# Kernel tuning notes

Measured on AMD Instinct MI355X. Metric: run time of the kernel, lower is better.

Reference implementation:

```python
import jax, jax.numpy as jnp
import numpy as np

B, T, C = 4, 2048, 768
N_HEAD = 12
HEAD_DIM = C // N_HEAD


def setup_inputs() -> dict:
    key = jax.random.key(0)
    k1, k2, k3 = jax.random.split(key, 3)
    x = jax.random.normal(k1, (B, T, C), dtype=jnp.float32)
    w_attn = jax.random.normal(k2, (C, 3 * C), dtype=jnp.float32) * (1.0 / np.sqrt(C))
    b_attn = jnp.zeros((3 * C,), dtype=jnp.float32)
    w_proj = jax.random.normal(k3, (C, C), dtype=jnp.float32) * (1.0 / np.sqrt(C))
    b_proj = jnp.zeros((C,), dtype=jnp.float32)
    return {"x": x, "w_attn": w_attn, "b_attn": b_attn, "w_proj": w_proj, "b_proj": b_proj}


def reference(x, w_attn, b_attn, w_proj, b_proj):
    # x: [B, T, C]
    Bs, Ts, Cs = x.shape
    qkv = x @ w_attn + b_attn                         # [B, T, 3C]
    q, k, v = jnp.split(qkv, 3, axis=-1)
    # -> [B, H, T, Dh]
    q = q.reshape(Bs, Ts, N_HEAD, HEAD_DIM).swapaxes(1, 2)
    k = k.reshape(Bs, Ts, N_HEAD, HEAD_DIM).swapaxes(1, 2)
    v = v.reshape(Bs, Ts, N_HEAD, HEAD_DIM).swapaxes(1, 2)
    scale = 1.0 / jnp.sqrt(jnp.asarray(HEAD_DIM, dtype=x.dtype))
    att = jnp.einsum('bhqd,bhkd->bhqk', q, k) * scale  # [B, H, T, T]
    causal = jnp.tril(jnp.ones((Ts, Ts), dtype=bool))[None, None]
    att = jnp.where(causal, att, jnp.asarray(-jnp.inf, dtype=att.dtype))
    att = jax.nn.softmax(att, axis=-1)
    y = jnp.einsum('bhqk,bhkd->bhqd', att, v)          # [B, H, T, Dh]
    y = y.swapaxes(1, 2).reshape(Bs, Ts, Cs)
    y = y @ w_proj + b_proj
    return y
```

## Files before the change

### kernel.cpp

```cpp
#include <hip/hip_runtime.h>
#include <cstdint>
#include <cstddef>

typedef __bf16 bf16x8 __attribute__((ext_vector_type(8)));
typedef float  f32x4  __attribute__((ext_vector_type(4)));
typedef unsigned short us;

#define DEV static __device__ __forceinline__

DEV us f2bf(float f) {
    unsigned int u = __builtin_bit_cast(unsigned int, f);
    u += 0x7FFFu + ((u >> 16) & 1u);
    return (us)(u >> 16);
}
DEV unsigned int pack2bf(float a, float b) {
    unsigned int ua = __builtin_bit_cast(unsigned int, a) + 0x8000u;
    unsigned int ub = __builtin_bit_cast(unsigned int, b) + 0x8000u;
    return (ua >> 16) | (ub & 0xFFFF0000u);
}

DEV void gll16(const void* g, void* l) {
    __builtin_amdgcn_global_load_lds(
        (const __attribute__((address_space(1))) unsigned int*)g,
        (__attribute__((address_space(3))) unsigned int*)l, 16, 0, 0);
}

DEV bf16x8 ld_frag(const us* p) {
    return __builtin_bit_cast(bf16x8, *reinterpret_cast<const uint4*>(p));
}

#define BB 4
#define TT 2048
#define CC 768
#define NH 12
#define DH 64
#define MM (BB*TT)
#define QSCALE 0.1803368801111144f

#define PREP_CAST_BLK 1024
#define PREP_TA_BLK   ((3*CC/32)*(CC/32))
#define PREP_TP_BLK   ((CC/32)*(CC/32))

__global__ __launch_bounds__(256)
void prep_k(const float* __restrict__ x, us* __restrict__ xb,
            const float* __restrict__ wA, us* __restrict__ wAt,
            const float* __restrict__ wP, us* __restrict__ wPt)
{
    const int bid = blockIdx.x;
    const int tid = threadIdx.x;

    if (bid < PREP_CAST_BLK) {
        const int n4 = MM * CC / 4;
        int i = bid * 256 + tid;
        const int stride = PREP_CAST_BLK * 256;
        for (; i < n4; i += stride) {
            float4 f = reinterpret_cast<const float4*>(x)[i];
            ushort4 o;
            o.x = f2bf(f.x); o.y = f2bf(f.y); o.z = f2bf(f.z); o.w = f2bf(f.w);
            reinterpret_cast<ushort4*>(xb)[i] = o;
        }
        return;
    }

    __shared__ float tile[32][33];
    const float* src; us* dst; int R, Cc, tb;
    if (bid < PREP_CAST_BLK + PREP_TA_BLK) {
        src = wA; dst = wAt; R = CC; Cc = 3 * CC; tb = bid - PREP_CAST_BLK;
    } else {
        src = wP; dst = wPt; R = CC; Cc = CC;     tb = bid - PREP_CAST_BLK - PREP_TA_BLK;
    }
    const int gx = Cc / 32;
    const int c0 = (tb % gx) * 32, r0 = (tb / gx) * 32;
    const int tx = tid & 31, ty = tid >> 5;
#pragma unroll
    for (int i = 0; i < 4; ++i)
        tile[ty + i*8][tx] = src[(size_t)(r0 + ty + i*8) * Cc + c0 + tx];
    __syncthreads();
#pragma unroll
    for (int i = 0; i < 4; ++i)
        dst[(size_t)(c0 + ty + i*8) * R + r0 + tx] = f2bf(tile[tx][ty + i*8]);
}


#define BM 128
#define BN 128
#define BK 32

template<int MODE>
__global__ __launch_bounds__(256)
void gemm_bt(const us* __restrict__ A,
             const us* __restrict__ Bt,
             const float* __restrict__ bias,
             float* __restrict__ Cout,
             us* __restrict__ Qo, us* __restrict__ Ko, us* __restrict__ Vo,
             int M, int N, int K)
{
    __shared__ __align__(16) us As[2][BM * BK];
    __shared__ __align__(16) us Bs[2][BN * BK];

    const int tid  = threadIdx.x;
    const int wave = tid >> 6, lane = tid & 63;
    const int quad = lane >> 4, l16 = lane & 15;
    const int waveM = (wave >> 1) * 64, waveN = (wave & 1) * 64;
    const int m0 = blockIdx.y * BM, n0 = blockIdx.x * BN;

    const f32x4 zero4 = {0.f, 0.f, 0.f, 0.f};
    f32x4 acc[4][4];
#pragma unroll
    for (int i = 0; i < 4; ++i)
#pragma unroll
        for (int j = 0; j < 4; ++j) acc[i][j] = zero4;

    const int lrow = lane >> 2, lch = (lane & 3) * 8;
    const int nk = K / BK;

    auto STAGE = [&](int buf, int kt) {
#pragma unroll
        for (int c = 0; c < 2; ++c) {
            int rb = (wave * 2 + c) * 16;
            int row = rb + lrow;
            gll16(A  + (size_t)(m0 + row) * K + kt * BK + lch, &As[buf][rb * BK]);
            gll16(Bt + (size_t)(n0 + row) * K + kt * BK + lch, &Bs[buf][rb * BK]);
        }
    };

    STAGE(0, 0);
    __syncthreads();
    int cur = 0;

    for (int kt = 0; kt < nk; ++kt) {
        if (kt + 1 < nk) STAGE(cur ^ 1, kt + 1);

        bf16x8 af[4], bfv[4];
#pragma unroll
        for (int mi = 0; mi < 4; ++mi)
            af[mi] = *reinterpret_cast<const bf16x8*>(&As[cur][(waveM + mi * 16 + l16) * BK + quad * 8]);
#pragma unroll
        for (int ni = 0; ni < 4; ++ni)
            bfv[ni] = *reinterpret_cast<const bf16x8*>(&Bs[cur][(waveN + ni * 16 + l16) * BK + quad * 8]);
#pragma unroll
        for (int mi = 0; mi < 4; ++mi)
#pragma unroll
            for (int ni = 0; ni < 4; ++ni)
                acc[mi][ni] = __builtin_amdgcn_mfma_f32_16x16x32_bf16(af[mi], bfv[ni], acc[mi][ni], 0, 0, 0);

        __syncthreads();
        cur ^= 1;
    }

#pragma unroll
    for (int mi = 0; mi < 4; ++mi) {
#pragma unroll
        for (int ni = 0; ni < 4; ++ni) {
            int n = n0 + waveN + ni * 16 + l16;
            float bv = bias[n];
            int mg = m0 + waveM + mi * 16 + quad * 4;
            if (MODE == 0) {
#pragma unroll
                for (int reg = 0; reg < 4; ++reg)
                    Cout[(size_t)(mg + reg) * N + n] = acc[mi][ni][reg] + bv;
            } else {
                int which = n / CC, c2 = n % CC;
                int h = c2 >> 6, d = c2 & 63;
                int b = mg >> 11, t0 = mg & 2047;
                size_t hb = (size_t)(b * NH + h) * TT * DH;
                if (which == 2) {
                    size_t off = hb + (size_t)(t0 >> 6) * 4096 + (d >> 4) * 1024
                               + ((t0 >> 3) & 7) * 128 + (d & 15) * 8 + (t0 & 7);
                    ushort4 pk;
                    pk.x = f2bf(acc[mi][ni][0] + bv);
                    pk.y = f2bf(acc[mi][ni][1] + bv);
                    pk.z = f2bf(acc[mi][ni][2] + bv);
                    pk.w = f2bf(acc[mi][ni][3] + bv);
                    *reinterpret_cast<ushort4*>(Vo + off) = pk;
                } else if (which == 1) {
                    size_t off = hb + (size_t)(t0 >> 4) * 1024 + (d >> 3) * 128
                               + (t0 & 15) * 8 + (d & 7);
#pragma unroll
                    for (int reg = 0; reg < 4; ++reg)
                        Ko[off + reg * 8] = f2bf(acc[mi][ni][reg] + bv);
                } else {
#pragma unroll
                    for (int reg = 0; reg < 4; ++reg) {
                        size_t off = hb + (size_t)(t0 + reg) * DH + d;
                        Qo[off] = f2bf((acc[mi][ni][reg] + bv) * QSCALE);
                    }
                }
            }
        }
    }
}

#define PST 72

__global__ __launch_bounds__(128)
void attn_k(const us* __restrict__ Qg,
            const us* __restrict__ Kg,
            const us* __restrict__ Vt,
            us* __restrict__ Og)
{
    __shared__ __align__(16) us Ps[2][32 * PST];

    const int tid  = threadIdx.x;
    const int wave = tid >> 6, lane = tid & 63;
    const int quad = lane >> 4, l16 = lane & 15;

    const int id  = blockIdx.x;
    const int xcd = id & 7, s = id >> 3;
    const int bh  = xcd + 8 * (s >> 4);
    const int q   = s & 15;
    const int pw  = 2 * q + wave;

    const size_t base = (size_t)bh * TT * DH;
    const int b = bh / NH, h = bh % NH;
    us* myP = Ps[wave];

    const f32x4 zero4 = {0.f, 0.f, 0.f, 0.f};

#pragma unroll 1
    for (int seg = 0; seg < 2; ++seg) {
        const int g   = seg ? 63 - pw : pw;
        const int nkt = (g >> 1) + 1;
        const int mA  = g * 32 + l16;
        const int mB  = mA + 16;

        bf16x8 qfA0 = ld_frag(Qg + base + (size_t)mA * DH + quad * 8);
        bf16x8 qfA1 = ld_frag(Qg + base + (size_t)mA * DH + 32 + quad * 8);
        bf16x8 qfB0 = ld_frag(Qg + base + (size_t)mB * DH + quad * 8);
        bf16x8 qfB1 = ld_frag(Qg + base + (size_t)mB * DH + 32 + quad * 8);

        f32x4 oA[4], oB[4];
#pragma unroll
        for (int i = 0; i < 4; ++i) { oA[i] = zero4; oB[i] = zero4; }
        float lrA = 0.f, lrB = 0.f;

#pragma unroll 1
        for (int j = 0; j < nkt; ++j) {
            const us* kb = Kg + base + (size_t)j * 4096;
            const us* vb = Vt + base + (size_t)j * 4096;

            bf16x8 kf[4][2];
#pragma unroll
            for (int sub = 0; sub < 4; ++sub)
#pragma unroll
                for (int hh = 0; hh < 2; ++hh)
                    kf[sub][hh] = ld_frag(kb + sub * 1024 + hh * 512 + lane * 8);

            f32x4 sA[4], sB[4];
#pragma unroll
            for (int sub = 0; sub < 4; ++sub) {
                f32x4 t = __builtin_amdgcn_mfma_f32_16x16x32_bf16(kf[sub][0], qfA0, zero4, 0, 0, 0);
                sA[sub]  = __builtin_amdgcn_mfma_f32_16x16x32_bf16(kf[sub][1], qfA1, t, 0, 0, 0);
                f32x4 u = __builtin_amdgcn_mfma_f32_16x16x32_bf16(kf[sub][0], qfB0, zero4, 0, 0, 0);
                sB[sub]  = __builtin_amdgcn_mfma_f32_16x16x32_bf16(kf[sub][1], qfB1, u, 0, 0, 0);
            }

            bf16x8 vf[4][2];
#pragma unroll
            for (int dsub = 0; dsub < 4; ++dsub)
#pragma unroll
                for (int kc = 0; kc < 2; ++kc)
                    vf[dsub][kc] = ld_frag(vb + dsub * 1024 + kc * 512 + lane * 8);

            if (j == nkt - 1) {
#pragma unroll
                for (int sub = 0; sub < 4; ++sub)
#pragma unroll
                    for (int reg = 0; reg < 4; ++reg) {
                        int key = j * 64 + sub * 16 + quad * 4 + reg;
                        if (key > mA) sA[sub][reg] = -INFINITY;
                        if (key > mB) sB[sub][reg] = -INFINITY;
                    }
            }

            {
                float rs = 0.f;
#pragma unroll
                for (int sub = 0; sub < 4; ++sub) {
                    float p0 = exp2f(sA[sub][0]), p1 = exp2f(sA[sub][1]);
                    float p2 = exp2f(sA[sub][2]), p3 = exp2f(sA[sub][3]);
                    rs += (p0 + p1) + (p2 + p3);
                    uint2 pk; pk.x = pack2bf(p0, p1); pk.y = pack2bf(p2, p3);
                    *reinterpret_cast<uint2*>(&myP[l16 * PST + sub * 16 + quad * 4]) = pk;
                }
                lrA += rs;
            }
            {
                float rs = 0.f;
#pragma unroll
                for (int sub = 0; sub < 4; ++sub) {
                    float p0 = exp2f(sB[sub][0]), p1 = exp2f(sB[sub][1]);
                    float p2 = exp2f(sB[sub][2]), p3 = exp2f(sB[sub][3]);
                    rs += (p0 + p1) + (p2 + p3);
                    uint2 pk; pk.x = pack2bf(p0, p1); pk.y = pack2bf(p2, p3);
                    *reinterpret_cast<uint2*>(&myP[(16 + l16) * PST + sub * 16 + quad * 4]) = pk;
                }
                lrB += rs;
            }

#pragma unroll
            for (int kc = 0; kc < 2; ++kc) {
                bf16x8 pfA = *reinterpret_cast<const bf16x8*>(&myP[l16 * PST + kc * 32 + quad * 8]);
                bf16x8 pfB = *reinterpret_cast<const bf16x8*>(&myP[(16 + l16) * PST + kc * 32 + quad * 8]);
#pragma unroll
                for (int d = 0; d < 4; ++d) {
                    oA[d] = __builtin_amdgcn_mfma_f32_16x16x32_bf16(vf[d][kc], pfA, oA[d], 0, 0, 0);
                    oB[d] = __builtin_amdgcn_mfma_f32_16x16x32_bf16(vf[d][kc], pfB, oB[d], 0, 0, 0);
                }
            }
        }

        lrA += __shfl_xor(lrA, 16); lrA += __shfl_xor(lrA, 32);
        lrB += __shfl_xor(lrB, 16); lrB += __shfl_xor(lrB, 32);

        const float invA = 1.f / lrA, invB = 1.f / lrB;
        us* orowA = Og + ((size_t)(b * TT + mA)) * CC + h * DH;
        us* orowB = Og + ((size_t)(b * TT + mB)) * CC + h * DH;
#pragma unroll
        for (int d = 0; d < 4; ++d) {
            uint2 pa, pb;
            pa.x = pack2bf(oA[d][0] * invA, oA[d][1] * invA);
            pa.y = pack2bf(oA[d][2] * invA, oA[d][3] * invA);
            pb.x = pack2bf(oB[d][0] * invB, oB[d][1] * invB);
            pb.y = pack2bf(oB[d][2] * invB, oB[d][3] * invB);
            *reinterpret_cast<uint2*>(orowA + d * 16 + quad * 4) = pa;
            *reinterpret_cast<uint2*>(orowB + d * 16 + quad * 4) = pb;
        }
    }
}

extern "C" void kernel_launch(void* const* d_in, const int* in_sizes, int n_in,
                              void* d_out, int out_size, void* d_ws, size_t ws_size,
                              hipStream_t stream)
{
    const float* x      = (const float*)d_in[0];
    const float* w_attn = (const float*)d_in[1];
    const float* b_attn = (const float*)d_in[2];
    const float* w_proj = (const float*)d_in[3];
    const float* b_proj = (const float*)d_in[4];
    float* out = (float*)d_out;

    char* ws = (char*)d_ws;
    size_t off = 0;
    auto alloc = [&](size_t bytes) {
        void* p = ws + off;
        off += (bytes + 255) & ~(size_t)255;
        return p;
    };
    us* wtA = (us*)alloc((size_t)(3 * CC) * CC * 2);
    us* wtP = (us*)alloc((size_t)CC * CC * 2);
    us* xb  = (us*)alloc((size_t)MM * CC * 2);
    us* Qb  = (us*)alloc((size_t)MM * CC * 2);
    us* Kb  = (us*)alloc((size_t)MM * CC * 2);
    us* Vtb = (us*)alloc((size_t)MM * CC * 2);
    us* att = (us*)alloc((size_t)MM * CC * 2);

    prep_k<<<PREP_CAST_BLK + PREP_TA_BLK + PREP_TP_BLK, 256, 0, stream>>>(
        x, xb, w_attn, wtA, w_proj, wtP);

    gemm_bt<1><<<dim3((3 * CC) / BN, MM / BM), 256, 0, stream>>>(
        xb, wtA, b_attn, nullptr, Qb, Kb, Vtb, MM, 3 * CC, CC);

    attn_k<<<dim3(16 * BB * NH), 128, 0, stream>>>(Qb, Kb, Vtb, att);

    gemm_bt<0><<<dim3(CC / BN, MM / BM), 256, 0, stream>>>(
        att, wtP, b_proj, out, nullptr, nullptr, nullptr, MM, CC, CC);

    (void)in_sizes; (void)n_in; (void)out_size; (void)ws_size;
}
```

Before: 222.6 us.

## Keep attention P in registers via 16x16x16 MFMA and swizzle GEMM blocks across XCDs

The attention kernel feeds the bf16 probability tile straight from registers into 16x16x16 bf16 MFMAs, whose accumulator layout matches the operand layout. This removes the LDS round trip (store P, reload as 8-wide fragments), and V is reloaded with a matching 4-element layout. Separately, both GEMMs switch to a 1D grid with an XCD-aware block swizzle so neighbouring tiles land on the same XCD for better L2 reuse. The trade-off is twice as many MFMA instructions, each half as deep, plus more, narrower V loads.

```diff
diff --git a/kernel.cpp b/kernel.cpp
--- a/kernel.cpp
+++ b/kernel.cpp
@@ -5,6 +5,20 @@
 typedef __bf16 bf16x8 __attribute__((ext_vector_type(8)));
 typedef float  f32x4  __attribute__((ext_vector_type(4)));
 typedef unsigned short us;
+
+#if defined(__has_builtin)
+#if __has_builtin(__builtin_amdgcn_mfma_f32_16x16x16bf16_1k)
+#define HAS_MFMA16 1
+#endif
+#endif
+#ifndef HAS_MFMA16
+#define HAS_MFMA16 0
+#endif
+
+#if HAS_MFMA16
+typedef short s16x4 __attribute__((ext_vector_type(4)));
+#define MFMA16(a, b, c) __builtin_amdgcn_mfma_f32_16x16x16bf16_1k(a, b, c, 0, 0, 0)
+#endif
 
 #define DEV static __device__ __forceinline__
 
@@ -102,7 +116,12 @@
     const int wave = tid >> 6, lane = tid & 63;
     const int quad = lane >> 4, l16 = lane & 15;
     const int waveM = (wave >> 1) * 64, waveN = (wave & 1) * 64;
-    const int m0 = blockIdx.y * BM, n0 = blockIdx.x * BN;
+
+    const int nxt   = N / BN;
+    const int chunk = gridDim.x >> 3;
+    const int lid   = blockIdx.x;
+    const int swz   = (lid & 7) * chunk + (lid >> 3);
+    const int m0 = (swz / nxt) * BM, n0 = (swz % nxt) * BN;
 
     const f32x4 zero4 = {0.f, 0.f, 0.f, 0.f};
     f32x4 acc[4][4];
@@ -199,7 +218,9 @@
             const us* __restrict__ Vt,
             us* __restrict__ Og)
 {
+#if !HAS_MFMA16
     __shared__ __align__(16) us Ps[2][32 * PST];
+#endif
 
     const int tid  = threadIdx.x;
     const int wave = tid >> 6, lane = tid & 63;
@@ -213,9 +234,14 @@
 
     const size_t base = (size_t)bh * TT * DH;
     const int b = bh / NH, h = bh % NH;
+#if !HAS_MFMA16
     us* myP = Ps[wave];
+#endif
 
     const f32x4 zero4 = {0.f, 0.f, 0.f, 0.f};
+#if HAS_MFMA16
+    const int vo = (quad >> 1) * 128 + l16 * 8 + (quad & 1) * 4;
+#endif
 
 #pragma unroll 1
     for (int seg = 0; seg < 2; ++seg) {
@@ -255,12 +281,22 @@
                 sB[sub]  = __builtin_amdgcn_mfma_f32_16x16x32_bf16(kf[sub][1], qfB1, u, 0, 0, 0);
             }
 
+#if HAS_MFMA16
+            s16x4 vreg[4][4];
+#pragma unroll
+            for (int sub = 0; sub < 4; ++sub)
+#pragma unroll
+                for (int dsub = 0; dsub < 4; ++dsub)
+                    vreg[sub][dsub] = __builtin_bit_cast(s16x4,
+                        *reinterpret_cast<const uint2*>(vb + dsub * 1024 + sub * 256 + vo));
+#else
             bf16x8 vf[4][2];
 #pragma unroll
             for (int dsub = 0; dsub < 4; ++dsub)
 #pragma unroll
                 for (int kc = 0; kc < 2; ++kc)
                     vf[dsub][kc] = ld_frag(vb + dsub * 1024 + kc * 512 + lane * 8);
+#endif
 
             if (j == nkt - 1) {
 #pragma unroll
@@ -273,6 +309,42 @@
                     }
             }
 
+#if HAS_MFMA16
+            uint2 pA16[4], pB16[4];
+            {
+                float rs = 0.f;
+#pragma unroll
+                for (int sub = 0; sub < 4; ++sub) {
+                    float p0 = exp2f(sA[sub][0]), p1 = exp2f(sA[sub][1]);
+                    float p2 = exp2f(sA[sub][2]), p3 = exp2f(sA[sub][3]);
+                    rs += (p0 + p1) + (p2 + p3);
+                    pA16[sub].x = pack2bf(p0, p1); pA16[sub].y = pack2bf(p2, p3);
+                }
+                lrA += rs;
+            }
+            {
+                float rs = 0.f;
+#pragma unroll
+                for (int sub = 0; sub < 4; ++sub) {
+                    float p0 = exp2f(sB[sub][0]), p1 = exp2f(sB[sub][1]);
+                    float p2 = exp2f(sB[sub][2]), p3 = exp2f(sB[sub][3]);
+                    rs += (p0 + p1) + (p2 + p3);
+                    pB16[sub].x = pack2bf(p0, p1); pB16[sub].y = pack2bf(p2, p3);
+                }
+                lrB += rs;
+            }
+
+#pragma unroll
+            for (int sub = 0; sub < 4; ++sub) {
+                s16x4 pa = __builtin_bit_cast(s16x4, pA16[sub]);
+                s16x4 pb = __builtin_bit_cast(s16x4, pB16[sub]);
+#pragma unroll
+                for (int dsub = 0; dsub < 4; ++dsub) {
+                    oA[dsub] = MFMA16(vreg[sub][dsub], pa, oA[dsub]);
+                    oB[dsub] = MFMA16(vreg[sub][dsub], pb, oB[dsub]);
+                }
+            }
+#else
             {
                 float rs = 0.f;
 #pragma unroll
@@ -297,7 +369,6 @@
                 }
                 lrB += rs;
             }
-
 #pragma unroll
             for (int kc = 0; kc < 2; ++kc) {
                 bf16x8 pfA = *reinterpret_cast<const bf16x8*>(&myP[l16 * PST + kc * 32 + quad * 8]);
@@ -308,6 +379,7 @@
                     oB[d] = __builtin_amdgcn_mfma_f32_16x16x32_bf16(vf[d][kc], pfB, oB[d], 0, 0, 0);
                 }
             }
+#endif
         }
 
         lrA += __shfl_xor(lrA, 16); lrA += __shfl_xor(lrA, 32);
@@ -358,12 +430,12 @@
     prep_k<<<PREP_CAST_BLK + PREP_TA_BLK + PREP_TP_BLK, 256, 0, stream>>>(
         x, xb, w_attn, wtA, w_proj, wtP);
 
-    gemm_bt<1><<<dim3((3 * CC) / BN, MM / BM), 256, 0, stream>>>(
+    gemm_bt<1><<<dim3((3 * CC) / BN * (MM / BM)), 256, 0, stream>>>(
         xb, wtA, b_attn, nullptr, Qb, Kb, Vtb, MM, 3 * CC, CC);
 
     attn_k<<<dim3(16 * BB * NH), 128, 0, stream>>>(Qb, Kb, Vtb, att);
 
-    gemm_bt<0><<<dim3(CC / BN, MM / BM), 256, 0, stream>>>(
+    gemm_bt<0><<<dim3((CC / BN) * (MM / BM)), 256, 0, stream>>>(
         att, wtP, b_proj, out, nullptr, nullptr, nullptr, MM, CC, CC);
 
     (void)in_sizes; (void)n_in; (void)out_size; (void)ws_size;
```

Result: no change. 224.8 us (+1.0%).
